# Kernel tuning notes

Measured on AMD Instinct MI355X. Metric: run time of the kernel, lower is better.

## Reference

```python
import jax, jax.numpy as jnp
import numpy as np

EMBED_DIM = 1024
NUM_HEADS = 16
HEAD_DIM = EMBED_DIM // NUM_HEADS
N, SEQ = 4, 2048


def setup_inputs() -> dict:
    key = jax.random.key(0)
    ks = jax.random.split(key, 9)
    s = 0.02
    return {
        "keys": jax.random.normal(ks[0], (N, SEQ, EMBED_DIM), jnp.float32),
        "values": jax.random.normal(ks[1], (N, SEQ, EMBED_DIM), jnp.float32),
        "queries": jax.random.normal(ks[2], (N, SEQ, EMBED_DIM), jnp.float32),
        "mask": jax.random.randint(ks[3], (N, 1, SEQ, SEQ), 0, 2, jnp.int32),
        "Wk": jax.random.normal(ks[4], (HEAD_DIM, HEAD_DIM), jnp.float32) * s,
        "Wv": jax.random.normal(ks[5], (HEAD_DIM, HEAD_DIM), jnp.float32) * s,
        "Wq": jax.random.normal(ks[6], (HEAD_DIM, HEAD_DIM), jnp.float32) * s,
        "Wo": jax.random.normal(ks[7], (EMBED_DIM, EMBED_DIM), jnp.float32) * s,
        "bo": jax.random.normal(ks[8], (EMBED_DIM,), jnp.float32) * s,
    }


def reference(keys, values, queries, mask, Wk, Wv, Wq, Wo, bo):
    n, key_len, _ = keys.shape
    value_len = values.shape[1]
    query_len = queries.shape[1]
    # Faithful to source: direct reshape (N, L, E) -> (N, H, L, D), no transpose.
    k = keys.reshape(n, NUM_HEADS, key_len, HEAD_DIM) @ Wk.T
    v = values.reshape(n, NUM_HEADS, value_len, HEAD_DIM) @ Wv.T
    q = queries.reshape(n, NUM_HEADS, query_len, HEAD_DIM) @ Wq.T
    # Scaled by sqrt(embed_dim) as in the original (not sqrt(head_dim)).
    energy = jnp.einsum('nhqd,nhkd->nhqk', q, k) / jnp.sqrt(jnp.float32(EMBED_DIM))
    energy = jnp.where(mask == 0, jnp.float32(-1e20), energy)
    attention = jax.nn.softmax(energy, axis=-1)
    att_out = jnp.einsum('nhql,nhld->nhqd', attention, v)
    att_out = att_out.reshape(n, query_len, NUM_HEADS * HEAD_DIM)
    return att_out @ Wo.T + bo
```

## Files before the change

### kernel.cpp

```cpp
#include <hip/hip_runtime.h>

#define SEQ 2048
#define HDIM 64
#define NH 16

typedef __bf16 bf16x8 __attribute__((ext_vector_type(8)));
typedef float f32x4 __attribute__((ext_vector_type(4)));
typedef unsigned short u16x8 __attribute__((ext_vector_type(8)));
typedef unsigned short u16x4 __attribute__((ext_vector_type(4)));
typedef _Float16 f16x4 __attribute__((ext_vector_type(4)));
typedef unsigned int u32x2 __attribute__((ext_vector_type(2)));
typedef unsigned long long u64;

__device__ __forceinline__ unsigned short f2bf(float f) {
  unsigned int u = __builtin_bit_cast(unsigned int, f);
  u = (u + 0x7FFFu + ((u >> 16) & 1u)) >> 16;
  return (unsigned short)u;
}

__device__ __forceinline__ bf16x8 cvt8(f32x4 a, f32x4 b) {
  u16x8 u;
  u[0] = f2bf(a[0]); u[1] = f2bf(a[1]); u[2] = f2bf(a[2]); u[3] = f2bf(a[3]);
  u[4] = f2bf(b[0]); u[5] = f2bf(b[1]); u[6] = f2bf(b[2]); u[7] = f2bf(b[3]);
  return __builtin_bit_cast(bf16x8, u);
}

__device__ __forceinline__ f32x4 mfma16(bf16x8 a, bf16x8 b, f32x4 c) {
  return __builtin_amdgcn_mfma_f32_16x16x32_bf16(a, b, c, 0, 0, 0);
}
__device__ __forceinline__ f32x4 mfma16h(f16x4 a, f16x4 b, f32x4 c) {
  return __builtin_amdgcn_mfma_f32_16x16x16f16(a, b, c, 0, 0, 0);
}

__device__ __forceinline__ f16x4 pk4h(float a, float b, float cc, float d) {
  auto h0 = __builtin_amdgcn_cvt_pkrtz(a, b);
  auto h1 = __builtin_amdgcn_cvt_pkrtz(cc, d);
  u32x2 u = { __builtin_bit_cast(unsigned int, h0),
              __builtin_bit_cast(unsigned int, h1) };
  return __builtin_bit_cast(f16x4, u);
}

#define QSCALE 0.045084220027780106f

__global__ __launch_bounds__(256) void qkv_proj(
    const float* __restrict__ keys, const float* __restrict__ values,
    const float* __restrict__ queries,
    const float* __restrict__ Wk, const float* __restrict__ Wv,
    const float* __restrict__ Wq,
    unsigned short* __restrict__ kb, unsigned short* __restrict__ vb,
    unsigned short* __restrict__ qb)
{
  __shared__ __attribute__((aligned(16))) unsigned short vt[4][64][72];

  const int which = blockIdx.y;
  const float* __restrict__ in = (which == 0) ? keys : (which == 1) ? values : queries;
  const float* __restrict__ W  = (which == 0) ? Wk   : (which == 1) ? Wv     : Wq;
  unsigned short* __restrict__ op = (which == 0) ? kb : (which == 1) ? vb : qb;
  const float osc = (which == 2) ? QSCALE : 1.0f;
  const bool asf16 = (which == 1);

  const int tid = threadIdx.x;
  const int w = tid >> 6, lane = tid & 63, c = lane & 15, quad = lane >> 4;

  bf16x8 aw[4][2];
  #pragma unroll
  for (int dt = 0; dt < 4; ++dt)
    #pragma unroll
    for (int hh = 0; hh < 2; ++hh) {
      const float* wr = W + (dt * 16 + c) * 64 + hh * 32 + quad * 8;
      aw[dt][hh] = cvt8(*(const f32x4*)wr, *(const f32x4*)(wr + 4));
    }

  const int m00 = blockIdx.x * 256 + w * 64;
  #pragma unroll
  for (int s = 0; s < 4; ++s) {
    const int m0 = m00 + s * 16;
    const float* xr = in + (size_t)(m0 + c) * 64;
    bf16x8 x0 = cvt8(*(const f32x4*)(xr + quad * 8), *(const f32x4*)(xr + quad * 8 + 4));
    bf16x8 x1 = cvt8(*(const f32x4*)(xr + 32 + quad * 8), *(const f32x4*)(xr + 36 + quad * 8));
    f32x4 acc[4] = {};
    #pragma unroll
    for (int dt = 0; dt < 4; ++dt) {
      acc[dt] = mfma16(aw[dt][0], x0, acc[dt]);
      acc[dt] = mfma16(aw[dt][1], x1, acc[dt]);
    }
    if (asf16) {
      #pragma unroll
      for (int dt = 0; dt < 4; ++dt) {
        u16x4 pk = __builtin_bit_cast(u16x4,
            pk4h(acc[dt][0], acc[dt][1], acc[dt][2], acc[dt][3]));
        #pragma unroll
        for (int r = 0; r < 4; ++r)
          vt[w][dt * 16 + quad * 4 + r][s * 16 + c] = pk[r];
      }
    } else {
      unsigned short* orow = op + (size_t)(m0 + c) * 64 + quad * 4;
      #pragma unroll
      for (int dt = 0; dt < 4; ++dt) {
        u16x4 pk;
        pk[0] = f2bf(acc[dt][0] * osc); pk[1] = f2bf(acc[dt][1] * osc);
        pk[2] = f2bf(acc[dt][2] * osc); pk[3] = f2bf(acc[dt][3] * osc);
        *(u16x4*)(orow + dt * 16) = pk;
      }
    }
  }

  if (asf16) {
    unsigned short* tb = op + (size_t)(m00 >> 11) * (64 * SEQ)
                            + (size_t)((m00 & 2047) >> 6) * (64 * 64);
    #pragma unroll
    for (int k = 0; k < 8; ++k) {
      const int row = k * 8 + (lane >> 3), colb = (lane & 7) * 8;
      u16x8 v = *(const u16x8*)&vt[w][row][colb];
      *(u16x8*)(tb + (size_t)row * 64 + colb) = v;
    }
  }
}

__global__ __launch_bounds__(256) void cvt_wo(const float* __restrict__ src,
                                              unsigned short* __restrict__ dst)
{
  int i = (blockIdx.x * 256 + threadIdx.x) * 4;
  f32x4 v = *reinterpret_cast<const f32x4*>(src + i);
  u16x4 o;
  o[0] = f2bf(v[0]); o[1] = f2bf(v[1]); o[2] = f2bf(v[2]); o[3] = f2bf(v[3]);
  *reinterpret_cast<u16x4*>(dst + i) = o;
}

__global__ __launch_bounds__(256) void maskpack(const int* __restrict__ mask,
                                                u64* __restrict__ bits)
{
  const int wid = blockIdx.x * 4 + (threadIdx.x >> 6);
  const int lane = threadIdx.x & 63;
  const int* src = mask + (size_t)wid * 1024 + lane;
  u64* dst = bits + (size_t)wid * 16;
  #pragma unroll
  for (int i = 0; i < 16; ++i) {
    u64 b = __ballot(src[i * 64] != 0);
    if (lane == 0) dst[i] = b;
  }
}

__global__ __launch_bounds__(256, 4) void attn4(
    const unsigned short* __restrict__ qb, const unsigned short* __restrict__ kb,
    const unsigned short* __restrict__ vb, const u64* __restrict__ mbits,
    unsigned short* __restrict__ att)
{
  __shared__ __attribute__((aligned(16))) unsigned short Kl[64][72];
  __shared__ __attribute__((aligned(16))) unsigned short Vt[64][72];
  __shared__ unsigned int mlut[16][2];

  const int tid = threadIdx.x;
  const int w = tid >> 6, lane = tid & 63, c = lane & 15, quad = lane >> 4;

  const int bid = blockIdx.x;
  const int xcd = bid & 7, rr = bid >> 3;
  const int qx = rr & 15, gh = rr >> 4;
  const int G = xcd + gh * 8;
  const int n = G >> 4;
  const int q0 = qx * 128;
  const size_t hb = (size_t)G * (SEQ * HDIM);

  if (tid < 16) {
    unsigned m = tid;
    mlut[m][0] = ((m & 1u) ? 0xFFFFu : 0u) | ((m & 2u) ? 0xFFFF0000u : 0u);
    mlut[m][1] = ((m & 4u) ? 0xFFFFu : 0u) | ((m & 8u) ? 0xFFFF0000u : 0u);
  }

  bf16x8 aq[2][2];
  #pragma unroll
  for (int qt = 0; qt < 2; ++qt) {
    const unsigned short* qr = qb + hb + (size_t)(q0 + qt * 64 + w * 16 + c) * HDIM;
    aq[qt][0] = *reinterpret_cast<const bf16x8*>(qr + quad * 8);
    aq[qt][1] = *reinterpret_cast<const bf16x8*>(qr + 32 + quad * 8);
  }

  f32x4 o[2][4] = {};
  f32x4 osum[2] = {};
  const f16x4 ones = {(_Float16)1.f, (_Float16)1.f, (_Float16)1.f, (_Float16)1.f};

  const u64* mb = mbits + ((size_t)n * SEQ + q0 + w * 16 + c) * 32;

  const bool isK = tid < 128;
  const int srow = (tid & 127) >> 1, scol = (tid & 1) * 32;
  const unsigned short* sptr = (isK ? kb : vb) + hb + (size_t)srow * 64 + scol;
  unsigned short (*Sl)[72] = isK ? Kl : Vt;

  u16x8 st0 = *(const u16x8*)(sptr);
  u16x8 st1 = *(const u16x8*)(sptr + 8);
  u16x8 st2 = *(const u16x8*)(sptr + 16);
  u16x8 st3 = *(const u16x8*)(sptr + 24);
  u64 mcur0 = mb[0];
  u64 mcur1 = mb[2048];

  for (int step = 0; step < 32; ++step) {
    __syncthreads();
    *(u16x8*)&Sl[srow][scol]      = st0;
    *(u16x8*)&Sl[srow][scol + 8]  = st1;
    *(u16x8*)&Sl[srow][scol + 16] = st2;
    *(u16x8*)&Sl[srow][scol + 24] = st3;
    u64 b0 = mcur0 >> (quad * 4);
    u64 b1 = mcur1 >> (quad * 4);
    if (step < 31) {
      const unsigned short* p = sptr + (size_t)(step + 1) * 4096;
      st0 = *(const u16x8*)(p);
      st1 = *(const u16x8*)(p + 8);
      st2 = *(const u16x8*)(p + 16);
      st3 = *(const u16x8*)(p + 24);
      mcur0 = mb[step + 1];
      mcur1 = mb[2048 + step + 1];
    }
    __syncthreads();

    f32x4 e[2][4] = {};
    #pragma unroll
    for (int t = 0; t < 4; ++t) {
      bf16x8 kf0 = *reinterpret_cast<const bf16x8*>(&Kl[t * 16 + c][quad * 8]);
      bf16x8 kf1 = *reinterpret_cast<const bf16x8*>(&Kl[t * 16 + c][32 + quad * 8]);
      #pragma unroll
      for (int qt = 0; qt < 2; ++qt) {
        e[qt][t] = mfma16(kf0, aq[qt][0], e[qt][t]);
        e[qt][t] = mfma16(kf1, aq[qt][1], e[qt][t]);
      }
    }

    f16x4 pf[2][4];
    #pragma unroll
    for (int qt = 0; qt < 2; ++qt) {
      u64 bb = qt ? b1 : b0;
      unsigned int lo = (unsigned int)bb, hi = (unsigned int)(bb >> 32);
      #pragma unroll
      for (int t = 0; t < 4; ++t) {
        unsigned int nib = (((t & 2) ? hi : lo) >> ((t & 1) * 16)) & 0xFu;
        f32x4 ev = e[qt][t];
        f16x4 pk = pk4h(__builtin_amdgcn_exp2f(ev[0]),
                        __builtin_amdgcn_exp2f(ev[1]),
                        __builtin_amdgcn_exp2f(ev[2]),
                        __builtin_amdgcn_exp2f(ev[3]));
        u32x2 pw = __builtin_bit_cast(u32x2, pk);
        pw[0] &= mlut[nib][0];
        pw[1] &= mlut[nib][1];
        pf[qt][t] = __builtin_bit_cast(f16x4, pw);
      }
    }

    __builtin_amdgcn_s_setprio(1);
    #pragma unroll
    for (int dt = 0; dt < 4; ++dt) {
      #pragma unroll
      for (int t = 0; t < 4; ++t) {
        f16x4 vf = __builtin_bit_cast(f16x4,
            *(const u16x4*)&Vt[dt * 16 + c][t * 16 + quad * 4]);
        o[0][dt] = mfma16h(vf, pf[0][t], o[0][dt]);
        o[1][dt] = mfma16h(vf, pf[1][t], o[1][dt]);
      }
    }
    #pragma unroll
    for (int t = 0; t < 4; ++t) {
      osum[0] = mfma16h(ones, pf[0][t], osum[0]);
      osum[1] = mfma16h(ones, pf[1][t], osum[1]);
    }
    __builtin_amdgcn_s_setprio(0);
  }

  #pragma unroll
  for (int qt = 0; qt < 2; ++qt) {
    float inv = 1.0f / osum[qt][0];
    unsigned short* orow =
        att + hb + (size_t)(q0 + qt * 64 + w * 16 + c) * HDIM + quad * 4;
    #pragma unroll
    for (int dt = 0; dt < 4; ++dt) {
      u16x4 pk = { f2bf(o[qt][dt][0] * inv), f2bf(o[qt][dt][1] * inv),
                   f2bf(o[qt][dt][2] * inv), f2bf(o[qt][dt][3] * inv) };
      *(u16x4*)(orow + dt * 16) = pk;
    }
  }
}

__global__ __launch_bounds__(256) void out_proj3(
    const unsigned short* __restrict__ att, const unsigned short* __restrict__ wob,
    const float* __restrict__ bo, float* __restrict__ out)
{
  __shared__ __attribute__((aligned(16))) unsigned short As[64][72];
  __shared__ __attribute__((aligned(16))) unsigned short Bs[128][72];

  const int nb = blockIdx.x, mbk = blockIdx.y;
  const int tid = threadIdx.x;
  const int w = tid >> 6, lane = tid & 63, c = lane & 15, quad = lane >> 4;
  const int wm = w & 1, wn = w >> 1;
  const int m0 = mbk * 64, n0 = nb * 128;
  const int arow = tid >> 2, acol = (tid & 3) * 16;
  const int brow = tid >> 1, bcol = (tid & 1) * 32;

  const unsigned short* sa = att + (size_t)(m0 + arow) * 1024 + acol;
  const unsigned short* sb = wob + (size_t)(n0 + brow) * 1024 + bcol;

  f32x4 acc[2][4] = {};

  u16x8 ra0 = *(const u16x8*)(sa);
  u16x8 ra1 = *(const u16x8*)(sa + 8);
  u16x8 rb0 = *(const u16x8*)(sb);
  u16x8 rb1 = *(const u16x8*)(sb + 8);
  u16x8 rb2 = *(const u16x8*)(sb + 16);
  u16x8 rb3 = *(const u16x8*)(sb + 24);

  for (int k0 = 0; k0 < 1024; k0 += 64) {
    __syncthreads();
    *(u16x8*)&As[arow][acol]          = ra0;
    *(u16x8*)&As[arow][acol + 8]      = ra1;
    *(u16x8*)&Bs[brow][bcol]          = rb0;
    *(u16x8*)&Bs[brow][bcol + 8]      = rb1;
    *(u16x8*)&Bs[brow][bcol + 16]     = rb2;
    *(u16x8*)&Bs[brow][bcol + 24]     = rb3;
    if (k0 < 960) {
      const unsigned short* pa = sa + k0 + 64;
      const unsigned short* pb = sb + k0 + 64;
      ra0 = *(const u16x8*)(pa);
      ra1 = *(const u16x8*)(pa + 8);
      rb0 = *(const u16x8*)(pb);
      rb1 = *(const u16x8*)(pb + 8);
      rb2 = *(const u16x8*)(pb + 16);
      rb3 = *(const u16x8*)(pb + 24);
    }
    __syncthreads();

    #pragma unroll
    for (int kk = 0; kk < 64; kk += 32) {
      bf16x8 af[2];
      #pragma unroll
      for (int mt = 0; mt < 2; ++mt)
        af[mt] = *reinterpret_cast<const bf16x8*>(&As[wm * 32 + mt * 16 + c][kk + quad * 8]);
      #pragma unroll
      for (int nt = 0; nt < 4; ++nt) {
        bf16x8 bf_ = *reinterpret_cast<const bf16x8*>(&Bs[wn * 64 + nt * 16 + c][kk + quad * 8]);
        #pragma unroll
        for (int mt = 0; mt < 2; ++mt)
          acc[mt][nt] = mfma16(af[mt], bf_, acc[mt][nt]);
      }
    }
  }

  #pragma unroll
  for (int nt = 0; nt < 4; ++nt) {
    const int col = n0 + wn * 64 + nt * 16 + c;
    const float bias = bo[col];
    #pragma unroll
    for (int mt = 0; mt < 2; ++mt)
      #pragma unroll
      for (int r = 0; r < 4; ++r)
        out[(size_t)(m0 + wm * 32 + mt * 16 + quad * 4 + r) * 1024 + col] =
            acc[mt][nt][r] + bias;
  }
}

extern "C" void kernel_launch(void* const* d_in, const int* in_sizes, int n_in,
                              void* d_out, int out_size, void* d_ws, size_t ws_size,
                              hipStream_t stream) {
  const float* keys    = (const float*)d_in[0];
  const float* values  = (const float*)d_in[1];
  const float* queries = (const float*)d_in[2];
  const int*   mask    = (const int*)d_in[3];
  const float* Wk      = (const float*)d_in[4];
  const float* Wv      = (const float*)d_in[5];
  const float* Wq      = (const float*)d_in[6];
  const float* Wo      = (const float*)d_in[7];
  const float* bo      = (const float*)d_in[8];
  float* out = (float*)d_out;

  const size_t T = (size_t)4 * NH * SEQ * HDIM;
  unsigned short* ws  = (unsigned short*)d_ws;
  unsigned short* kb  = ws;
  unsigned short* vb  = kb + T;
  unsigned short* qb  = vb + T;
  unsigned short* att = qb + T;
  unsigned short* wob = att + T;
  u64* mbits = (u64*)(wob + 1024 * 1024);

  qkv_proj<<<dim3(512, 3), 256, 0, stream>>>(keys, values, queries,
                                             Wk, Wv, Wq, kb, vb, qb);
  cvt_wo<<<dim3(1024), 256, 0, stream>>>(Wo, wob);
  maskpack<<<dim3(4096), 256, 0, stream>>>(mask, mbits);
  attn4<<<dim3(1024), 256, 0, stream>>>(qb, kb, vb, mbits, att);
  out_proj3<<<dim3(8, 128), 256, 0, stream>>>(att, wob, bo, out);
}
```

Measured before the change: 346.7 us.

## Enlarge out-projection tile to 128x128 with XCD-aware block mapping

The output projection GEMM now computes a 128x128 tile per block instead of 64x128, so each wave holds a 4x4 grid of MFMA accumulators. This doubles the reuse of each B fragment and halves the number of blocks. The grid is flattened to 1D, and block ids are remapped so blocks sharing an M row stripe land on the same XCD, which is meant to improve L2 reuse of the A tiles. The larger accumulator state raises register pressure and leaves fewer blocks to spread across the CUs.

```diff
diff --git a/kernel.cpp b/kernel.cpp
--- a/kernel.cpp
+++ b/kernel.cpp
@@ -277,28 +277,32 @@
   }
 }
 
-__global__ __launch_bounds__(256) void out_proj3(
+__global__ __launch_bounds__(256) void out_proj4(
     const unsigned short* __restrict__ att, const unsigned short* __restrict__ wob,
     const float* __restrict__ bo, float* __restrict__ out)
 {
-  __shared__ __attribute__((aligned(16))) unsigned short As[64][72];
+  __shared__ __attribute__((aligned(16))) unsigned short As[128][72];
   __shared__ __attribute__((aligned(16))) unsigned short Bs[128][72];
 
-  const int nb = blockIdx.x, mbk = blockIdx.y;
+  const int bid = blockIdx.x;
+  const int xcd = bid & 7, rr = bid >> 3;
+  const int nb = rr & 7, g = rr >> 3;
+  const int mbk = xcd + g * 8;
   const int tid = threadIdx.x;
   const int w = tid >> 6, lane = tid & 63, c = lane & 15, quad = lane >> 4;
   const int wm = w & 1, wn = w >> 1;
-  const int m0 = mbk * 64, n0 = nb * 128;
-  const int arow = tid >> 2, acol = (tid & 3) * 16;
-  const int brow = tid >> 1, bcol = (tid & 1) * 32;
-
-  const unsigned short* sa = att + (size_t)(m0 + arow) * 1024 + acol;
-  const unsigned short* sb = wob + (size_t)(n0 + brow) * 1024 + bcol;
-
-  f32x4 acc[2][4] = {};
+  const int m0 = mbk * 128, n0 = nb * 128;
+  const int srow = tid >> 1, scol = (tid & 1) * 32;
+
+  const unsigned short* sa = att + (size_t)(m0 + srow) * 1024 + scol;
+  const unsigned short* sb = wob + (size_t)(n0 + srow) * 1024 + scol;
+
+  f32x4 acc[4][4] = {};
 
   u16x8 ra0 = *(const u16x8*)(sa);
   u16x8 ra1 = *(const u16x8*)(sa + 8);
+  u16x8 ra2 = *(const u16x8*)(sa + 16);
+  u16x8 ra3 = *(const u16x8*)(sa + 24);
   u16x8 rb0 = *(const u16x8*)(sb);
   u16x8 rb1 = *(const u16x8*)(sb + 8);
   u16x8 rb2 = *(const u16x8*)(sb + 16);
@@ -306,37 +310,38 @@
 
   for (int k0 = 0; k0 < 1024; k0 += 64) {
     __syncthreads();
-    *(u16x8*)&As[arow][acol]          = ra0;
-    *(u16x8*)&As[arow][acol + 8]      = ra1;
-    *(u16x8*)&Bs[brow][bcol]          = rb0;
-    *(u16x8*)&Bs[brow][bcol + 8]      = rb1;
-    *(u16x8*)&Bs[brow][bcol + 16]     = rb2;
-    *(u16x8*)&Bs[brow][bcol + 24]     = rb3;
+    *(u16x8*)&As[srow][scol]      = ra0;
+    *(u16x8*)&As[srow][scol + 8]  = ra1;
+    *(u16x8*)&As[srow][scol + 16] = ra2;
+    *(u16x8*)&As[srow][scol + 24] = ra3;
+    *(u16x8*)&Bs[srow][scol]      = rb0;
+    *(u16x8*)&Bs[srow][scol + 8]  = rb1;
+    *(u16x8*)&Bs[srow][scol + 16] = rb2;
+    *(u16x8*)&Bs[srow][scol + 24] = rb3;
     if (k0 < 960) {
       const unsigned short* pa = sa + k0 + 64;
       const unsigned short* pb = sb + k0 + 64;
-      ra0 = *(const u16x8*)(pa);
-      ra1 = *(const u16x8*)(pa + 8);
-      rb0 = *(const u16x8*)(pb);
-      rb1 = *(const u16x8*)(pb + 8);
-      rb2 = *(const u16x8*)(pb + 16);
-      rb3 = *(const u16x8*)(pb + 24);
+      ra0 = *(const u16x8*)(pa);      ra1 = *(const u16x8*)(pa + 8);
+      ra2 = *(const u16x8*)(pa + 16); ra3 = *(const u16x8*)(pa + 24);
+      rb0 = *(const u16x8*)(pb);      rb1 = *(const u16x8*)(pb + 8);
+      rb2 = *(const u16x8*)(pb + 16); rb3 = *(const u16x8*)(pb + 24);
     }
     __syncthreads();
 
     #pragma unroll
     for (int kk = 0; kk < 64; kk += 32) {
-      bf16x8 af[2];
-      #pragma unroll
-      for (int mt = 0; mt < 2; ++mt)
-        af[mt] = *reinterpret_cast<const bf16x8*>(&As[wm * 32 + mt * 16 + c][kk + quad * 8]);
-      #pragma unroll
-      for (int nt = 0; nt < 4; ++nt) {
-        bf16x8 bf_ = *reinterpret_cast<const bf16x8*>(&Bs[wn * 64 + nt * 16 + c][kk + quad * 8]);
+      bf16x8 af[4], bfr[4];
+      #pragma unroll
+      for (int mt = 0; mt < 4; ++mt)
+        af[mt] = *reinterpret_cast<const bf16x8*>(&As[wm * 64 + mt * 16 + c][kk + quad * 8]);
+      #pragma unroll
+      for (int nt = 0; nt < 4; ++nt)
+        bfr[nt] = *reinterpret_cast<const bf16x8*>(&Bs[wn * 64 + nt * 16 + c][kk + quad * 8]);
+      #pragma unroll
+      for (int nt = 0; nt < 4; ++nt)
         #pragma unroll
-        for (int mt = 0; mt < 2; ++mt)
-          acc[mt][nt] = mfma16(af[mt], bf_, acc[mt][nt]);
-      }
+        for (int mt = 0; mt < 4; ++mt)
+          acc[mt][nt] = mfma16(af[mt], bfr[nt], acc[mt][nt]);
     }
   }
 
@@ -345,10 +350,10 @@
     const int col = n0 + wn * 64 + nt * 16 + c;
     const float bias = bo[col];
     #pragma unroll
-    for (int mt = 0; mt < 2; ++mt)
+    for (int mt = 0; mt < 4; ++mt)
       #pragma unroll
       for (int r = 0; r < 4; ++r)
-        out[(size_t)(m0 + wm * 32 + mt * 16 + quad * 4 + r) * 1024 + col] =
+        out[(size_t)(m0 + wm * 64 + mt * 16 + quad * 4 + r) * 1024 + col] =
             acc[mt][nt][r] + bias;
   }
 }
@@ -381,5 +386,5 @@
   cvt_wo<<<dim3(1024), 256, 0, stream>>>(Wo, wob);
   maskpack<<<dim3(4096), 256, 0, stream>>>(mask, mbits);
   attn4<<<dim3(1024), 256, 0, stream>>>(qb, kb, vb, mbits, att);
-  out_proj3<<<dim3(8, 128), 256, 0, stream>>>(att, wob, bo, out);
-}
+  out_proj4<<<dim3(512), 256, 0, stream>>>(att, wob, bo, out);
+}
```

Measured after the change: 339.4 us, median of 2. 1.02x faster.
